# Performance work log

Measured on AMD Instinct MI355X. Metric: run time of the kernel, lower is better.

The kernel has to match this reference:

```python
import jax, jax.numpy as jnp
import numpy as np
from jax import lax

INF = 1e10
R = 20          # max_distance: EDT truncated at this radius (exact under clamp)
NUM_CLASSES = 19


def _pass1d(f, axis):
    """1D squared distance transform min_{|d|<=R} (d^2 + f[shifted]), truncated.
    f: [..., H, W] with 0 at 'source' pixels, INF elsewhere. Out-of-bounds = INF
    (matches scipy, which sees nothing beyond the array border)."""
    pad = [(0, 0)] * f.ndim
    pad[axis] = (R, R)
    fp = jnp.pad(f, pad, constant_values=INF)
    n = f.shape[axis]
    out = jnp.full_like(f, INF)
    for d in range(2 * R + 1):  # fixed small loop (41 iters), jit-unrolled
        shifted = lax.slice_in_dim(fp, d, d + n, axis=axis)
        out = jnp.minimum(out, shifted + float((d - R) ** 2))
    return out


def edt_trunc(mask):
    """Euclidean distance from each True pixel to nearest False pixel,
    truncated at R (False pixels get 0). mask: [..., H, W] bool."""
    f = jnp.where(mask, INF, 0.0).astype(jnp.float32)
    g = _pass1d(f, -2)
    g = _pass1d(g, -1)
    return jnp.sqrt(jnp.minimum(g, float(R * R)))


def compute_sdf(onehot_bool):
    """Signed distance: negdist - posdist, per [B,C,H,W] one-hot masks.
    Already truncated at +-R, matching clamp(-R, R) in the torch module."""
    posdist = edt_trunc(onehot_bool)    # distance inside FG to BG
    negdist = edt_trunc(~onehot_bool)   # distance inside BG to FG
    return negdist - posdist


def setup_inputs() -> dict:
    key = jax.random.key(0)
    k1, k2 = jax.random.split(key)
    logits = jax.random.normal(k1, (8, NUM_CLASSES, 256, 512), dtype=jnp.float32)
    targets = jax.random.randint(k2, (8, 256, 512), 0, NUM_CLASSES, dtype=jnp.int64)
    return {"logits": logits, "targets": targets}


def reference(logits, targets):
    C = logits.shape[1]
    probs = jax.nn.softmax(logits, axis=1)                       # [B,C,H,W]
    onehot = jax.nn.one_hot(targets, C, axis=1, dtype=jnp.bool_)  # [B,C,H,W]
    sdf = compute_sdf(onehot)
    sdf = jnp.clip(sdf, -float(R), float(R)) / float(R)
    # mean over spatial, sum over classes, mean over batch (reduction='mean')
    per_class = jnp.mean(probs * sdf, axis=(2, 3))               # [B,C]
    loss = jnp.sum(per_class, axis=1)                            # [B]
    return jnp.mean(loss)
```

## Files before the change

### kernel.cpp

```cpp
#include <hip/hip_runtime.h>
#include <hip/hip_bf16.h>
#include <math.h>

#define NCLS 19
#define BB   8
#define HH   256
#define WW   512
#define CAP2 400u
#define SEG  8
#define VROW 576

typedef unsigned short u16x2 __attribute__((ext_vector_type(2)));

static __device__ __forceinline__ unsigned umin32(unsigned a, unsigned b) { return a < b ? a : b; }
static __device__ __forceinline__ float fsqrt_fast(float x) { return __builtin_amdgcn_sqrtf(x); }

static __device__ __forceinline__ unsigned pk_add_s(unsigned v, unsigned c) {
    unsigned d; asm("v_pk_add_u16 %0, %1, %2" : "=v"(d) : "s"(c), "v"(v)); return d;
}
static __device__ __forceinline__ unsigned pk_minv(unsigned a, unsigned b) {
    unsigned d; asm("v_pk_min_u16 %0, %1, %2" : "=v"(d) : "v"(a), "v"(b)); return d;
}
static __device__ __forceinline__ unsigned pk_maxv(unsigned a, unsigned b) {
    unsigned d; asm("v_pk_max_u16 %0, %1, %2" : "=v"(d) : "v"(a), "v"(b)); return d;
}
static __device__ __forceinline__ unsigned pk_hmin(unsigned a) {
    unsigned d;
    asm("v_pk_min_u16 %0, %1, %1 op_sel:[1,0] op_sel_hi:[0,1]" : "=v"(d) : "v"(a));
    return d;
}

__global__ __launch_bounds__(256)
void kA_vert(const int* __restrict__ targ, unsigned short* __restrict__ vsq,
             unsigned long long* __restrict__ acc) {
    if (blockIdx.x == 0 && threadIdx.x == 0) { *acc = 0ULL; }
    int gid = blockIdx.x * 256 + threadIdx.x;

    for (int i = gid; i < BB * NCLS * HH * 64; i += 131072) {
        int p = i & 63;
        int rch = i >> 6;
        vsq[(size_t)rch * VROW + ((p < 32) ? p : (512 + p))] = 441;
    }

    int col = gid & 4095;
    int seg = gid >> 12;
    int b = col >> 9;
    int w = col & 511;
    int h0 = seg * SEG;
    const int* tp = &targ[b * HH * WW + w];

    unsigned d[NCLS];
    unsigned pk[NCLS][2];
#pragma unroll
    for (int c = 0; c < NCLS; ++c) { d[c] = 21u; pk[c][0] = 0u; pk[c][1] = 0u; }
#pragma unroll
    for (int k = 0; k < 21 + SEG; ++k) {
        int hh = h0 - 21 + k;
        int t = -1;
        if (hh >= 0) t = tp[hh * WW];
#pragma unroll
        for (int c = 0; c < NCLS; ++c)
            d[c] = (t == c) ? 0u : d[c] + 1u;
        if (k >= 21) {
            int r = k - 21;
#pragma unroll
            for (int c = 0; c < NCLS; ++c)
                pk[c][r >> 2] |= d[c] << ((r & 3) * 8);
        }
    }
    unsigned u[NCLS];
#pragma unroll
    for (int c = 0; c < NCLS; ++c) u[c] = 21u;
#pragma unroll
    for (int k = 0; k < 21 + SEG; ++k) {
        int hh = h0 + 21 + SEG - 1 - k;
        int t = -1;
        if (hh < HH) t = tp[hh * WW];
#pragma unroll
        for (int c = 0; c < NCLS; ++c)
            u[c] = (t == c) ? 0u : u[c] + 1u;
        if (k >= 21) {
            int r = 21 + SEG - 1 - k;
#pragma unroll
            for (int c = 0; c < NCLS; ++c) {
                unsigned dv = (pk[c][r >> 2] >> ((r & 3) * 8)) & 0xffu;
                unsigned m = umin32(dv, u[c]);
                vsq[((size_t)(b * NCLS + c) * HH + hh) * VROW + 32 + w] =
                    (unsigned short)(m * m);
            }
        }
    }
}

__global__ __launch_bounds__(256)
void kB_main(const float* __restrict__ logits,
             const unsigned short* __restrict__ vsq,
             unsigned long long* __restrict__ acc) {
    __shared__ float sNum[4][256];
    __shared__ float sDen[4][256];
    __shared__ float sEt[4][256];
    __shared__ unsigned short sM2[4][256];
    __shared__ float wsum[4];
    int tid = threadIdx.x;
    int L = tid & 63;
    int wid = tid >> 6;
    int bh = blockIdx.x;
    int b = bh >> 8;
    int h = bh & 255;

#define SQx(x) ((unsigned)((x) * (x)))
#define PK2(a, bq) (SQx(a) | (SQx(bq) << 16))
    const unsigned CE[21] = {
        PK2(-20,-19), PK2(-18,-17), PK2(-16,-15), PK2(-14,-13), PK2(-12,-11),
        PK2(-10,-9),  PK2(-8,-7),   PK2(-6,-5),   PK2(-4,-3),   PK2(-2,-1),
        PK2(0,1),     PK2(2,3),     PK2(4,5),     PK2(6,7),     PK2(8,9),
        PK2(10,11),   PK2(12,13),   PK2(14,15),   PK2(16,17),   PK2(18,19),
        PK2(20,21) };
    const unsigned CO[21] = {
        PK2(-21,-20), PK2(-19,-18), PK2(-17,-16), PK2(-15,-14), PK2(-13,-12),
        PK2(-11,-10), PK2(-9,-8),   PK2(-7,-6),   PK2(-5,-4),   PK2(-3,-2),
        PK2(-1,0),    PK2(1,2),     PK2(3,4),     PK2(5,6),     PK2(7,8),
        PK2(9,10),    PK2(11,12),   PK2(13,14),   PK2(15,16),   PK2(17,18),
        PK2(19,20) };
#undef PK2
#undef SQx

    const unsigned short* vbase =
        vsq + ((size_t)(b * NCLS + wid) * HH + h) * VROW + 8 + 8 * L;
    const float* lroww = &logits[((size_t)(b * NCLS + wid) * HH + h) * WW + 8 * L];
    int nc = (wid < 3) ? 5 : 4;

    float den[8], num[8], et[8];
    unsigned m2[8];
#pragma unroll
    for (int p = 0; p < 8; ++p) { den[p]=0.f; num[p]=0.f; et[p]=0.f; m2[p]=0xFFFFu; }

    float4 f0n = *(const float4*)lroww;
    float4 f1n = *(const float4*)(lroww + 4);

#pragma unroll 1
    for (int i = 0; i < nc; ++i) {
        float4 f0 = f0n, f1 = f1n;
        if (i + 1 < nc) {
            const float* ln = lroww + (size_t)(i + 1) * 4 * (HH * WW);
            f0n = *(const float4*)ln;
            f1n = *(const float4*)(ln + 4);
        }

        const uint4* wq = (const uint4*)(vbase + (size_t)(4 * i) * (HH * VROW));
        uint4 q0 = wq[0], q1 = wq[1], q2 = wq[2], q3 = wq[3],
              q4 = wq[4], q5 = wq[5], q6 = wq[6];
        unsigned W[28] = {q0.x,q0.y,q0.z,q0.w, q1.x,q1.y,q1.z,q1.w,
                          q2.x,q2.y,q2.z,q2.w, q3.x,q3.y,q3.z,q3.w,
                          q4.x,q4.y,q4.z,q4.w, q5.x,q5.y,q5.z,q5.w,
                          q6.x,q6.y,q6.z,q6.w};

        unsigned ae[4], ao[4];
#pragma unroll
        for (int r = 0; r < 4; ++r) { ae[r] = 0xFFFFFFFFu; ao[r] = 0xFFFFFFFFu; }

#pragma unroll
        for (int r = 0; r < 4; ++r)
#pragma unroll
            for (int m = 7; m <= 13; ++m) {
                ae[r] = pk_minv(ae[r], pk_add_s(W[r + m + 2], CE[m]));
                ao[r] = pk_minv(ao[r], pk_add_s(W[r + m + 2], CO[m]));
            }

        unsigned mx = pk_maxv(pk_maxv(pk_maxv(pk_hmin(ae[0]), pk_hmin(ao[0])),
                                      pk_maxv(pk_hmin(ae[1]), pk_hmin(ao[1]))),
                              pk_maxv(pk_maxv(pk_hmin(ae[2]), pk_hmin(ao[2])),
                                      pk_maxv(pk_hmin(ae[3]), pk_hmin(ao[3]))));
        if (!__all(mx <= (49u | (49u << 16)))) {
#pragma unroll
            for (int r = 0; r < 4; ++r) {
#pragma unroll
                for (int m = 0; m <= 6; ++m) {
                    ae[r] = pk_minv(ae[r], pk_add_s(W[r + m + 2], CE[m]));
                    ao[r] = pk_minv(ao[r], pk_add_s(W[r + m + 2], CO[m]));
                }
#pragma unroll
                for (int m = 14; m <= 20; ++m) {
                    ae[r] = pk_minv(ae[r], pk_add_s(W[r + m + 2], CE[m]));
                    ao[r] = pk_minv(ao[r], pk_add_s(W[r + m + 2], CO[m]));
                }
            }
        }

        float fx[8] = {f0.x, f0.y, f0.z, f0.w, f1.x, f1.y, f1.z, f1.w};
#pragma unroll
        for (int r = 0; r < 4; ++r) {
            unsigned nd0 = pk_hmin(ae[r]) & 0xFFFFu;
            unsigned nd1 = pk_hmin(ao[r]) & 0xFFFFu;
            float e0 = __expf(fx[2 * r]), e1 = __expf(fx[2 * r + 1]);
            den[2 * r] += e0; den[2 * r + 1] += e1;
            float s0 = fsqrt_fast((float)umin32(nd0, CAP2));
            float s1 = fsqrt_fast((float)umin32(nd1, CAP2));
            num[2 * r]     += e0 * s0;
            num[2 * r + 1] += e1 * s1;
            bool z0 = (nd0 == 0), z1 = (nd1 == 0);
            et[2 * r]     = z0 ? e0 : et[2 * r];
            et[2 * r + 1] = z1 ? e1 : et[2 * r + 1];
            m2[2 * r]     = umin32(m2[2 * r],     z0 ? 0xFFFFu : nd0);
            m2[2 * r + 1] = umin32(m2[2 * r + 1], z1 ? 0xFFFFu : nd1);
        }
    }

    float vsum = 0.f;
#pragma unroll
    for (int pass = 0; pass < 2; ++pass) {
        if ((L >> 5) == pass) {
            int base = 8 * (L & 31);
            *(float4*)&sNum[wid][base]     = (float4){num[0], num[1], num[2], num[3]};
            *(float4*)&sNum[wid][base + 4] = (float4){num[4], num[5], num[6], num[7]};
            *(float4*)&sDen[wid][base]     = (float4){den[0], den[1], den[2], den[3]};
            *(float4*)&sDen[wid][base + 4] = (float4){den[4], den[5], den[6], den[7]};
            *(float4*)&sEt[wid][base]      = (float4){et[0], et[1], et[2], et[3]};
            *(float4*)&sEt[wid][base + 4]  = (float4){et[4], et[5], et[6], et[7]};
            uint4 mq;
            mq.x = m2[0] | (m2[1] << 16); mq.y = m2[2] | (m2[3] << 16);
            mq.z = m2[4] | (m2[5] << 16); mq.w = m2[6] | (m2[7] << 16);
            *(uint4*)&sM2[wid][base] = mq;
        }
        __syncthreads();
        {
            float N = sNum[0][tid] + sNum[1][tid] + sNum[2][tid] + sNum[3][tid];
            float D = sDen[0][tid] + sDen[1][tid] + sDen[2][tid] + sDen[3][tid];
            float E = sEt[0][tid] + sEt[1][tid] + sEt[2][tid] + sEt[3][tid];
            unsigned M = umin32(umin32((unsigned)sM2[0][tid], (unsigned)sM2[1][tid]),
                                umin32((unsigned)sM2[2][tid], (unsigned)sM2[3][tid]));
            vsum += (N - E * fsqrt_fast((float)umin32(M, CAP2))) / D;
        }
        __syncthreads();
    }

#pragma unroll
    for (int off = 32; off >= 1; off >>= 1) vsum += __shfl_down(vsum, off);
    if (L == 0) wsum[wid] = vsum;
    __syncthreads();
    if (tid == 0) {
        float s = (wsum[0] + wsum[1]) + (wsum[2] + wsum[3]);
        double q = (double)s * (68719476736.0 / 20.0);
        atomicAdd(acc, (unsigned long long)(long long)q);
    }
}

__global__ void kC_final(const unsigned long long* __restrict__ acc,
                         float* __restrict__ out) {
    long long iv = (long long)*acc;
    double v = (double)iv / 68719476736.0;
    out[0] = (float)(v / (double)((size_t)BB * HH * WW));
}

extern "C" void kernel_launch(void* const* d_in, const int* in_sizes, int n_in,
                              void* d_out, int out_size, void* d_ws, size_t ws_size,
                              hipStream_t stream) {
    const float* logits = (const float*)d_in[0];
    const int* targ = (const int*)d_in[1];
    unsigned char* wsb = (unsigned char*)d_ws;
    unsigned long long* acc = (unsigned long long*)wsb;
    unsigned short* vsq = (unsigned short*)(wsb + 64);

    kA_vert<<<512, 256, 0, stream>>>(targ, vsq, acc);
    kB_main<<<BB * HH, 256, 0, stream>>>(logits, vsq, acc);
    kC_final<<<1, 1, 0, stream>>>(acc, (float*)d_out);
}
```

Measured before the change: 65.26 us.

## Store vertical distances as bytes and stage squared rows with halo in LDS

The vertical pass now writes unsquared 8-bit distances instead of padded 16-bit squared values, and it no longer writes halo padding to global memory. The main kernel loads each class row as bytes, squares the values with packed 16-bit multiplies, and stores them in shared memory with the 441 halo filled there. The windowed min reads then come from LDS instead of global memory. This roughly halves the intermediate traffic and removes the halo-fill loop, at the cost of extra LDS (about 21KB per block), which may lower occupancy.

```diff
diff --git a/kernel.cpp b/kernel.cpp
--- a/kernel.cpp
+++ b/kernel.cpp
@@ -8,7 +8,7 @@
 #define WW   512
 #define CAP2 400u
 #define SEG  8
-#define VROW 576
+#define WPC  70
 
 typedef unsigned short u16x2 __attribute__((ext_vector_type(2)));
 
@@ -29,19 +29,22 @@
     asm("v_pk_min_u16 %0, %1, %1 op_sel:[1,0] op_sel_hi:[0,1]" : "=v"(d) : "v"(a));
     return d;
 }
+static __device__ __forceinline__ void sq8(unsigned x, unsigned& w0, unsigned& w1) {
+    unsigned a = x & 0x00FF00FFu;
+    unsigned b = (x >> 8) & 0x00FF00FFu;
+    u16x2 sa = __builtin_bit_cast(u16x2, a); sa = sa * sa;
+    u16x2 sb = __builtin_bit_cast(u16x2, b); sb = sb * sb;
+    unsigned ua = __builtin_bit_cast(unsigned, sa);
+    unsigned ub = __builtin_bit_cast(unsigned, sb);
+    w0 = __builtin_amdgcn_perm(ub, ua, 0x05040100u);
+    w1 = __builtin_amdgcn_perm(ub, ua, 0x07060302u);
+}
 
 __global__ __launch_bounds__(256)
-void kA_vert(const int* __restrict__ targ, unsigned short* __restrict__ vsq,
+void kA_vert(const int* __restrict__ targ, unsigned char* __restrict__ vneg,
              unsigned long long* __restrict__ acc) {
     if (blockIdx.x == 0 && threadIdx.x == 0) { *acc = 0ULL; }
     int gid = blockIdx.x * 256 + threadIdx.x;
-
-    for (int i = gid; i < BB * NCLS * HH * 64; i += 131072) {
-        int p = i & 63;
-        int rch = i >> 6;
-        vsq[(size_t)rch * VROW + ((p < 32) ? p : (512 + p))] = 441;
-    }
-
     int col = gid & 4095;
     int seg = gid >> 12;
     int b = col >> 9;
@@ -84,9 +87,8 @@
 #pragma unroll
             for (int c = 0; c < NCLS; ++c) {
                 unsigned dv = (pk[c][r >> 2] >> ((r & 3) * 8)) & 0xffu;
-                unsigned m = umin32(dv, u[c]);
-                vsq[((size_t)(b * NCLS + c) * HH + hh) * VROW + 32 + w] =
-                    (unsigned short)(m * m);
+                vneg[((size_t)(b * NCLS + c) * HH + hh) * WW + w] =
+                    (unsigned char)umin32(dv, u[c]);
             }
         }
     }
@@ -94,13 +96,15 @@
 
 __global__ __launch_bounds__(256)
 void kB_main(const float* __restrict__ logits,
-             const unsigned short* __restrict__ vsq,
+             const unsigned char* __restrict__ vneg,
              unsigned long long* __restrict__ acc) {
+    __shared__ uint4 lds4[NCLS * WPC];
     __shared__ float sNum[4][256];
     __shared__ float sDen[4][256];
     __shared__ float sEt[4][256];
     __shared__ unsigned short sM2[4][256];
     __shared__ float wsum[4];
+    unsigned* lds = (unsigned*)lds4;
     int tid = threadIdx.x;
     int L = tid & 63;
     int wid = tid >> 6;
@@ -125,11 +129,22 @@
 #undef PK2
 #undef SQx
 
-    const unsigned short* vbase =
-        vsq + ((size_t)(b * NCLS + wid) * HH + h) * VROW + 8 + 8 * L;
+    const unsigned HALO2 = 441u | (441u << 16);
     const float* lroww = &logits[((size_t)(b * NCLS + wid) * HH + h) * WW + 8 * L];
     int nc = (wid < 3) ? 5 : 4;
 
+#pragma unroll 1
+    for (int i = 0; i < nc; ++i) {
+        int c = wid + 4 * i;
+        uint2 v8 = ((const uint2*)vneg)[((size_t)(b * NCLS + c) * HH + h) * 64 + L];
+        uint4 wq;
+        sq8(v8.x, wq.x, wq.y);
+        sq8(v8.y, wq.z, wq.w);
+        lds4[c * WPC + L + 3] = wq;
+        if (L < 12) lds[c * 280 + L] = HALO2;
+        if (L >= 52) lds[c * 280 + 216 + L] = HALO2;
+    }
+
     float den[8], num[8], et[8];
     unsigned m2[8];
 #pragma unroll
@@ -140,6 +155,7 @@
 
 #pragma unroll 1
     for (int i = 0; i < nc; ++i) {
+        int c = wid + 4 * i;
         float4 f0 = f0n, f1 = f1n;
         if (i + 1 < nc) {
             const float* ln = lroww + (size_t)(i + 1) * 4 * (HH * WW);
@@ -147,9 +163,9 @@
             f1n = *(const float4*)(ln + 4);
         }
 
-        const uint4* wq = (const uint4*)(vbase + (size_t)(4 * i) * (HH * VROW));
-        uint4 q0 = wq[0], q1 = wq[1], q2 = wq[2], q3 = wq[3],
-              q4 = wq[4], q5 = wq[5], q6 = wq[6];
+        const uint4* basep = &lds4[c * WPC + L];
+        uint4 q0 = basep[0], q1 = basep[1], q2 = basep[2], q3 = basep[3],
+              q4 = basep[4], q5 = basep[5], q6 = basep[6];
         unsigned W[28] = {q0.x,q0.y,q0.z,q0.w, q1.x,q1.y,q1.z,q1.w,
                           q2.x,q2.y,q2.z,q2.w, q3.x,q3.y,q3.z,q3.w,
                           q4.x,q4.y,q4.z,q4.w, q5.x,q5.y,q5.z,q5.w,
@@ -259,9 +275,9 @@
     const int* targ = (const int*)d_in[1];
     unsigned char* wsb = (unsigned char*)d_ws;
     unsigned long long* acc = (unsigned long long*)wsb;
-    unsigned short* vsq = (unsigned short*)(wsb + 64);
-
-    kA_vert<<<512, 256, 0, stream>>>(targ, vsq, acc);
-    kB_main<<<BB * HH, 256, 0, stream>>>(logits, vsq, acc);
+    unsigned char* vneg = wsb + 64;
+
+    kA_vert<<<512, 256, 0, stream>>>(targ, vneg, acc);
+    kB_main<<<BB * HH, 256, 0, stream>>>(logits, vneg, acc);
     kC_final<<<1, 1, 0, stream>>>(acc, (float*)d_out);
 }
```

New measurement: 63.01 us. 3.4% less time.
